# Kernel tuning notes

Hardware: AMD Instinct MI355X
Metric: run time of the kernel (lower is better)

## Reference

```python
import jax, jax.numpy as jnp
import numpy as np

B, C_IN, H, W = 16, 256, 64, 64
D, K = 128, 1024  # embed_dim, nb_entries


def setup_inputs() -> dict:
    key = jax.random.key(0)
    k1, k2, k3, k4 = jax.random.split(key, 4)
    x = jax.random.normal(k1, (B, C_IN, H, W), dtype=jnp.float32)
    conv_w = jax.random.normal(k2, (C_IN, D), dtype=jnp.float32) * 0.05
    conv_b = jax.random.normal(k3, (D,), dtype=jnp.float32) * 0.05
    embed = jax.random.normal(k4, (D, K), dtype=jnp.float32)
    return {"x": x, "conv_w": conv_w, "conv_b": conv_b, "embed": embed}


def reference(x, conv_w, conv_b, embed):
    # 1x1 conv == per-pixel matmul; go straight to NHWC layout.
    z = jnp.einsum('bchw,cd->bhwd', x, conv_w) + conv_b        # [B,H,W,D]
    flat = z.reshape(-1, D)                                     # [N,D]
    # Squared-euclidean distances to codebook columns (||f||^2 - 2 f.E + ||e||^2).
    dist = (jnp.sum(flat * flat, axis=1, keepdims=True)
            - 2.0 * (flat @ embed)
            + jnp.sum(embed * embed, axis=0, keepdims=True))    # [N,K]
    embed_ind = jnp.argmin(dist, axis=1)                        # [N] int
    embed_ind = embed_ind.reshape(B, H, W)
    quantize = jnp.take(embed.T, embed_ind, axis=0)             # [B,H,W,D] gather
    diff = jnp.mean((jax.lax.stop_gradient(quantize) - z) ** 2)
    quantize = z + jax.lax.stop_gradient(quantize - z)          # straight-through
    return quantize.transpose(0, 3, 1, 2), diff, embed_ind
```

## Files before the change

kernel.cpp:

```cpp
#include <hip/hip_runtime.h>

typedef __attribute__((ext_vector_type(4))) float f32x4;
typedef __attribute__((ext_vector_type(8))) short bf16x8;

constexpr int CIN = 256;
constexpr int D   = 128;
constexpr int K   = 1024;
constexpr int HW  = 4096;
constexpr int MT  = 128;
constexpr int DIFF_OFF = 8388608;
constexpr int IDX_OFF  = 8388609;

__device__ float g_scratch[16 + K];
__device__ __align__(16) uint4 g_efrags[64 * 4 * 64];
__device__ __align__(16) uint4 g_wfrags[8 * 8 * 3 * 64];
__device__ __align__(16) float g_embedT[K * D];

__device__ inline unsigned short f2bf(float f) {
    unsigned u = __float_as_uint(f);
    u = u + 0x7fff + ((u >> 16) & 1);
    return (unsigned short)(u >> 16);
}
__device__ inline float bf2f(unsigned short h) {
    return __uint_as_float(((unsigned)h) << 16);
}
__device__ inline void split3(float v, short& a, short& b, short& c) {
    unsigned short h = f2bf(v); float r1 = v - bf2f(h);
    unsigned short m = f2bf(r1); float r2 = r1 - bf2f(m);
    a = (short)h; b = (short)m; c = (short)f2bf(r2);
}
__device__ inline void split3t(float v, short& a, short& b, short& c) {
    unsigned u1 = __float_as_uint(v) & 0xffff0000u;
    float r1 = v - __uint_as_float(u1);
    unsigned u2 = __float_as_uint(r1) & 0xffff0000u;
    float r2 = r1 - __uint_as_float(u2);
    a = (short)(u1 >> 16); b = (short)(u2 >> 16);
    c = (short)(__float_as_uint(r2) >> 16);
}
__device__ inline float med3f(float a, float b, float c) {
    float d;
    asm("v_med3_f32 %0, %1, %2, %3" : "=v"(d) : "v"(a), "v"(b), "v"(c));
    return d;
}
__device__ inline float min3f(float a, float b, float c) {
    float d;
    asm("v_min3_f32 %0, %1, %2, %3" : "=v"(d) : "v"(a), "v"(b), "v"(c));
    return d;
}
__device__ inline float packk(float s, int kk) {
    return __uint_as_float((__float_as_uint(s) & 0xFFFFFC00u) | (unsigned)kk);
}

__device__ inline void gload_lds16(const uint4* g, uint4* l) {
    __builtin_amdgcn_global_load_lds(
        (const __attribute__((address_space(1))) unsigned int*)g,
        (__attribute__((address_space(3))) unsigned int*)l,
        16, 0, 0);
}

__global__ void vq_prep_all(const float* __restrict__ embed,
                            const float* __restrict__ conv_w) {
    const int bi = blockIdx.x;
    const int t  = threadIdx.x;
    if (bi < 128) {
        __shared__ float tile[32][33];
        int kb = bi >> 2, db = bi & 3;
        int tk = t & 31, td = t >> 5;
        #pragma unroll
        for (int dd = 0; dd < 4; ++dd)
            tile[td * 4 + dd][tk] =
                embed[(size_t)(db * 32 + td * 4 + dd) * K + kb * 32 + tk];
        __syncthreads();
        #pragma unroll
        for (int dd = 0; dd < 4; ++dd)
            g_embedT[(size_t)(kb * 32 + td * 4 + dd) * D + db * 32 + tk] =
                tile[tk][td * 4 + dd];
    } else if (bi < 192) {
        int kt = bi - 128, dc = t >> 6, l = t & 63;
        int k  = kt * 16 + (l & 15);
        int d0 = dc * 32 + (l >> 4) * 8;
        unsigned short hi[8];
        #pragma unroll
        for (int j = 0; j < 8; ++j)
            hi[j] = f2bf(embed[(size_t)(d0 + j) * K + k]);
        uint4 H;
        H.x = (unsigned)hi[0] | ((unsigned)hi[1] << 16);
        H.y = (unsigned)hi[2] | ((unsigned)hi[3] << 16);
        H.z = (unsigned)hi[4] | ((unsigned)hi[5] << 16);
        H.w = (unsigned)hi[6] | ((unsigned)hi[7] << 16);
        g_efrags[(kt * 4 + dc) * 64 + l] = H;
    } else if (bi < 208) {
        int old = (bi - 192) * 4 + (t >> 6), l = t & 63;
        int cb = old >> 3, db = old & 7;
        int c0 = cb * 32 + (l >> 4) * 8, d = db * 16 + (l & 15);
        short s1[8], s2[8], s3[8];
        #pragma unroll
        for (int j = 0; j < 8; ++j)
            split3(conv_w[(size_t)(c0 + j) * D + d], s1[j], s2[j], s3[j]);
        #pragma unroll
        for (int s = 0; s < 3; ++s) {
            const short* sp = s == 0 ? s1 : s == 1 ? s2 : s3;
            uint4 P;
            P.x = (unsigned)(unsigned short)sp[0] | ((unsigned)(unsigned short)sp[1] << 16);
            P.y = (unsigned)(unsigned short)sp[2] | ((unsigned)(unsigned short)sp[3] << 16);
            P.z = (unsigned)(unsigned short)sp[4] | ((unsigned)(unsigned short)sp[5] << 16);
            P.w = (unsigned)(unsigned short)sp[6] | ((unsigned)(unsigned short)sp[7] << 16);
            g_wfrags[((cb * 8 + db) * 3 + s) * 64 + l] = P;
        }
    } else {
        int k = (bi - 208) * 256 + t;
        if (k == 0) g_scratch[0] = 0.0f;
        float s = 0.0f;
        for (int d = 0; d < D; ++d) { float v = embed[d * K + k]; s += v * v; }
        g_scratch[16 + k] = s;
    }
}

#define MFMA(a, bb, c) __builtin_amdgcn_mfma_f32_16x16x32_bf16(a, bb, c, 0, 0, 0)

__global__ __launch_bounds__(256, 2) void vq_main(
    const float* __restrict__ x, const float* __restrict__ conv_b,
    float* __restrict__ out)
{
    __shared__ __align__(16) uint4 ebuf[4096];
    __shared__ float e2_s[K];
    __shared__ float tbuf[4 * 16 * 36];
    __shared__ int   ks_s[MT];
    __shared__ float red_s[4];

    const int t    = threadIdx.x;
    const int lane = t & 63;
    const int w    = t >> 6;
    const int wg   = blockIdx.x;
    const int n0   = wg * MT;
    const int b    = n0 >> 12;
    const int hw0  = n0 & 4095;
    const int pxb  = w * 32;
    const int lp   = lane & 15;
    const int lg   = lane >> 4;
    const float INF = __uint_as_float(0x7f800000u);

    for (int k = t; k < K; k += 256) e2_s[k] = g_scratch[16 + k];

    f32x4 Cz[2][8];
    #pragma unroll
    for (int db = 0; db < 8; ++db) {
        float bv = conv_b[db * 16 + lp];
        Cz[0][db] = (f32x4){bv, bv, bv, bv};
        Cz[1][db] = Cz[0][db];
    }
    {
        #pragma unroll
        for (int i = 0; i < 6; ++i)
            gload_lds16(&g_wfrags[(w * 6 + i) * 64 + lane], &ebuf[(w * 6 + i) * 64]);
        asm volatile("s_waitcnt vmcnt(0)" ::: "memory");
        __syncthreads();

        const float* xl = x + (size_t)b * CIN * HW + (size_t)(lg * 8) * HW
                          + hw0 + pxb + lp;
        for (int cb = 0; cb < 8; ++cb) {
            float v[2][8];
            #pragma unroll
            for (int rb = 0; rb < 2; ++rb)
                #pragma unroll
                for (int j = 0; j < 8; ++j)
                    v[rb][j] = xl[(size_t)(cb * 32 + j) * HW + rb * 16];
            if (cb < 7) {
                const uint4* wsrc = g_wfrags + (size_t)(cb + 1) * 1536;
                uint4* wdst = ebuf + ((cb + 1) & 1) * 1536;
                #pragma unroll
                for (int i = 0; i < 6; ++i)
                    gload_lds16(&wsrc[(w * 6 + i) * 64 + lane], &wdst[(w * 6 + i) * 64]);
            }
            bf16x8 X1[2], X2[2], X3[2];
            #pragma unroll
            for (int rb = 0; rb < 2; ++rb)
                #pragma unroll
                for (int j = 0; j < 8; ++j) {
                    short a, bb, c;
                    split3t(v[rb][j], a, bb, c);
                    X1[rb][j] = a; X2[rb][j] = bb; X3[rb][j] = c;
                }
            const uint4* wb = ebuf + (cb & 1) * 1536;
            #pragma unroll
            for (int db = 0; db < 8; ++db) {
                bf16x8 W1 = *(const bf16x8*)&wb[(db * 3 + 0) * 64 + lane];
                bf16x8 W2 = *(const bf16x8*)&wb[(db * 3 + 1) * 64 + lane];
                bf16x8 W3 = *(const bf16x8*)&wb[(db * 3 + 2) * 64 + lane];
                Cz[0][db] = MFMA(X1[0], W1, Cz[0][db]);
                Cz[1][db] = MFMA(X1[1], W1, Cz[1][db]);
                Cz[0][db] = MFMA(X1[0], W2, Cz[0][db]);
                Cz[1][db] = MFMA(X1[1], W2, Cz[1][db]);
                Cz[0][db] = MFMA(X2[0], W1, Cz[0][db]);
                Cz[1][db] = MFMA(X2[1], W1, Cz[1][db]);
                Cz[0][db] = MFMA(X1[0], W3, Cz[0][db]);
                Cz[1][db] = MFMA(X1[1], W3, Cz[1][db]);
                Cz[0][db] = MFMA(X2[0], W2, Cz[0][db]);
                Cz[1][db] = MFMA(X2[1], W2, Cz[1][db]);
                Cz[0][db] = MFMA(X3[0], W1, Cz[0][db]);
                Cz[1][db] = MFMA(X3[1], W1, Cz[1][db]);
            }
            asm volatile("s_waitcnt vmcnt(0)" ::: "memory");
            __syncthreads();
        }
    }

    bf16x8 A2h[2][4];
    {
        float* tb = tbuf + w * 576;
        #pragma unroll
        for (int rb = 0; rb < 2; ++rb) {
            #pragma unroll
            for (int dc = 0; dc < 4; ++dc) {
                #pragma unroll
                for (int h = 0; h < 2; ++h)
                    #pragma unroll
                    for (int r = 0; r < 4; ++r)
                        tb[(lg * 4 + r) * 36 + h * 16 + lp] = Cz[rb][dc * 2 + h][r];
                asm volatile("s_waitcnt lgkmcnt(0)" ::: "memory");
                f32x4 a0 = *(const f32x4*)&tb[lp * 36 + lg * 8];
                f32x4 a1 = *(const f32x4*)&tb[lp * 36 + lg * 8 + 4];
                #pragma unroll
                for (int j = 0; j < 8; ++j)
                    A2h[rb][dc][j] = (short)f2bf(-2.0f * (j < 4 ? a0[j] : a1[j - 4]));
                asm volatile("s_waitcnt lgkmcnt(0)" ::: "memory");
            }
        }
    }

    const uint4* gfr = g_efrags;
    {
        #pragma unroll
        for (int i = 0; i < 8; ++i)
            gload_lds16(&gfr[(w * 8 + i) * 64 + lane], &ebuf[(w * 8 + i) * 64]);
        asm volatile("s_waitcnt vmcnt(0)" ::: "memory");
        __syncthreads();
    }

    float v1[8], v2[8], v3[8], v4[8];
    #pragma unroll
    for (int q = 0; q < 8; ++q) { v1[q] = INF; v2[q] = INF; v3[q] = INF; v4[q] = INF; }

    for (int c = 0; c < 8; ++c) {
        if (c < 7) {
            const uint4* esrc = gfr + (size_t)(c + 1) * 2048;
            uint4* edst = ebuf + ((c + 1) & 1) * 2048;
            #pragma unroll
            for (int i = 0; i < 8; ++i)
                gload_lds16(&esrc[(w * 8 + i) * 64 + lane], &edst[(w * 8 + i) * 64]);
        }
        const bf16x8* eb = (const bf16x8*)&ebuf[(c & 1) * 2048];
        #pragma unroll
        for (int ktl = 0; ktl < 8; ++ktl) {
            int kt = c * 8 + ktl;
            bf16x8 Bh[4];
            #pragma unroll
            for (int dc = 0; dc < 4; ++dc)
                Bh[dc] = eb[(ktl * 4 + dc) * 64 + lane];
            float e2v = e2_s[kt * 16 + lp] + 512.0f;
            f32x4 C0 = (f32x4){e2v, e2v, e2v, e2v};
            f32x4 C1 = C0;
            __builtin_amdgcn_s_setprio(1);
            #pragma unroll
            for (int dc = 0; dc < 4; ++dc) {
                C0 = MFMA(A2h[0][dc], Bh[dc], C0);
                C1 = MFMA(A2h[1][dc], Bh[dc], C1);
            }
            __builtin_amdgcn_s_setprio(0);
            int kk = kt * 16 + lp;
            #pragma unroll
            for (int rb = 0; rb < 2; ++rb) {
                f32x4 C = rb ? C1 : C0;
                #pragma unroll
                for (int r = 0; r < 4; ++r) {
                    int q = rb * 4 + r;
                    float s = packk(C[r], kk);
                    float t1 = fminf(v1[q], s);
                    float t2 = med3f(s, v1[q], v2[q]);
                    float t3 = med3f(s, v2[q], v3[q]);
                    float t4 = med3f(s, v3[q], v4[q]);
                    v1[q] = t1; v2[q] = t2; v3[q] = t3; v4[q] = t4;
                }
            }
        }
        if (c < 7) {
            asm volatile("s_waitcnt vmcnt(0)" ::: "memory");
            __syncthreads();
        }
    }

    float dacc = 0.0f;
    #pragma unroll
    for (int q = 0; q < 8; ++q) {
        const int rb = q >> 2, r = q & 3;
        float a1 = v1[q], a2 = v2[q], a3 = v3[q], a4 = v4[q], a5 = INF, a6 = INF;
        #pragma unroll
        for (int off = 1; off < 16; off <<= 1) {
            float b1 = __shfl_xor(a1, off), b2 = __shfl_xor(a2, off);
            float b3 = __shfl_xor(a3, off), b4 = __shfl_xor(a4, off);
            float b5 = __shfl_xor(a5, off), b6 = __shfl_xor(a6, off);
            float m11 = fmaxf(a1, b1);
            float m12 = fmaxf(a1, b2), m21 = fmaxf(a2, b1);
            float m13 = fmaxf(a1, b3), m22 = fmaxf(a2, b2), m31 = fmaxf(a3, b1);
            float m14 = fmaxf(a1, b4), m23 = fmaxf(a2, b3), m32 = fmaxf(a3, b2), m41 = fmaxf(a4, b1);
            float m15 = fmaxf(a1, b5), m24 = fmaxf(a2, b4), m33 = fmaxf(a3, b3), m42 = fmaxf(a4, b2), m51 = fmaxf(a5, b1);
            float c1 = fminf(a1, b1);
            float c2 = min3f(a2, b2, m11);
            float c3 = min3f(m12, m21, fminf(a3, b3));
            float c4 = fminf(min3f(a4, b4, m13), fminf(m22, m31));
            float c5 = fminf(min3f(a5, b5, m14), min3f(m23, m32, m41));
            float c6 = fminf(fminf(min3f(a6, b6, m15), min3f(m24, m33, m42)), m51);
            a1 = c1; a2 = c2; a3 = c3; a4 = c4; a5 = c5; a6 = c6;
        }
        float cm[6] = {a1, a2, a3, a4, a5, a6};
        float bd = 0.0f; int bk = 0;
        #pragma unroll
        for (int j = 0; j < 6; ++j) {
            int kc = (int)(__float_as_uint(cm[j]) & 1023u);
            float sum = 0.0f;
            #pragma unroll
            for (int db = 0; db < 8; ++db)
                sum += Cz[rb][db][r] * g_embedT[(size_t)kc * D + db * 16 + lp];
            #pragma unroll
            for (int off = 1; off < 16; off <<= 1) sum += __shfl_xor(sum, off);
            float de = e2_s[kc] - 2.0f * sum;
            if (j == 0) { bd = de; bk = kc; }
            else {
                bool upd = (de < bd) || (de == bd && kc < bk);
                bd = upd ? de : bd;
                bk = upd ? kc : bk;
            }
        }
        #pragma unroll
        for (int db = 0; db < 8; ++db) {
            float qv = g_embedT[(size_t)bk * D + db * 16 + lp];
            float df = qv - Cz[rb][db][r];
            dacc += df * df;
        }
        if (lp == 0) {
            int px = pxb + rb * 16 + lg * 4 + r;
            ks_s[px] = bk;
            out[IDX_OFF + n0 + px] = (float)bk;
        }
    }
    #pragma unroll
    for (int off = 1; off <= 32; off <<= 1) dacc += __shfl_xor(dacc, off);
    if (lane == 0) red_s[w] = dacc;
    __syncthreads();

    {
        int px = t & 127, half = t >> 7;
        int ks = ks_s[px];
        const f32x4* ep = (const f32x4*)&g_embedT[(size_t)ks * D + half * 64];
        float* ob = out + (size_t)b * D * HW + hw0 + px;
        #pragma unroll
        for (int d4 = 0; d4 < 16; ++d4) {
            f32x4 q4 = ep[d4];
            int d = half * 64 + d4 * 4;
            #pragma unroll
            for (int cc = 0; cc < 4; ++cc)
                ob[(size_t)(d + cc) * HW] = q4[cc];
        }
    }
    if (t == 0) atomicAdd(&g_scratch[0], red_s[0] + red_s[1] + red_s[2] + red_s[3]);
}

__global__ void vq_final(float* __restrict__ out) {
    out[DIFF_OFF] = g_scratch[0] / 8388608.0f;
}

extern "C" void kernel_launch(void* const* d_in, const int* in_sizes, int n_in,
                              void* d_out, int out_size, void* d_ws, size_t ws_size,
                              hipStream_t stream) {
    const float* x      = (const float*)d_in[0];
    const float* conv_w = (const float*)d_in[1];
    const float* conv_b = (const float*)d_in[2];
    const float* embed  = (const float*)d_in[3];
    float* out = (float*)d_out;

    vq_prep_all<<<212, 256, 0, stream>>>(embed, conv_w);
    vq_main    <<<512, 256, 0, stream>>>(x, conv_b, out);
    vq_final   <<<1,   1,   0, stream>>>(out);
}
```

Measured before the change: 84.89 us.

## Halve pixel tile per block, double grid, and stream W3 fragments from global

Result: slower. 121.2 us (+42.7%).

```diff
diff --git a/kernel.cpp b/kernel.cpp
--- a/kernel.cpp
+++ b/kernel.cpp
@@ -7,7 +7,7 @@
 constexpr int D   = 128;
 constexpr int K   = 1024;
 constexpr int HW  = 4096;
-constexpr int MT  = 128;
+constexpr int MT  = 64;
 constexpr int DIFF_OFF = 8388608;
 constexpr int IDX_OFF  = 8388609;
 
@@ -118,11 +118,11 @@
 
 #define MFMA(a, bb, c) __builtin_amdgcn_mfma_f32_16x16x32_bf16(a, bb, c, 0, 0, 0)
 
-__global__ __launch_bounds__(256, 2) void vq_main(
+__global__ __launch_bounds__(256, 3) void vq_main(
     const float* __restrict__ x, const float* __restrict__ conv_b,
     float* __restrict__ out)
 {
-    __shared__ __align__(16) uint4 ebuf[4096];
+    __shared__ __align__(16) uint4 ebuf[2048];
     __shared__ float e2_s[K];
     __shared__ float tbuf[4 * 16 * 36];
     __shared__ int   ks_s[MT];
@@ -135,155 +135,140 @@
     const int n0   = wg * MT;
     const int b    = n0 >> 12;
     const int hw0  = n0 & 4095;
-    const int pxb  = w * 32;
+    const int pxb  = w * 16;
     const int lp   = lane & 15;
     const int lg   = lane >> 4;
     const float INF = __uint_as_float(0x7f800000u);
 
     for (int k = t; k < K; k += 256) e2_s[k] = g_scratch[16 + k];
 
-    f32x4 Cz[2][8];
+    f32x4 Cz[8];
     #pragma unroll
     for (int db = 0; db < 8; ++db) {
         float bv = conv_b[db * 16 + lp];
-        Cz[0][db] = (f32x4){bv, bv, bv, bv};
-        Cz[1][db] = Cz[0][db];
+        Cz[db] = (f32x4){bv, bv, bv, bv};
     }
     {
         #pragma unroll
-        for (int i = 0; i < 6; ++i)
-            gload_lds16(&g_wfrags[(w * 6 + i) * 64 + lane], &ebuf[(w * 6 + i) * 64]);
+        for (int ii = 0; ii < 4; ++ii) {
+            int bi = w * 4 + ii;
+            gload_lds16(&g_wfrags[(((bi >> 1)) * 3 + (bi & 1)) * 64 + lane],
+                        &ebuf[bi * 64]);
+        }
         asm volatile("s_waitcnt vmcnt(0)" ::: "memory");
         __syncthreads();
 
         const float* xl = x + (size_t)b * CIN * HW + (size_t)(lg * 8) * HW
                           + hw0 + pxb + lp;
         for (int cb = 0; cb < 8; ++cb) {
-            float v[2][8];
-            #pragma unroll
-            for (int rb = 0; rb < 2; ++rb)
+            float v[8];
+            #pragma unroll
+            for (int j = 0; j < 8; ++j)
+                v[j] = xl[(size_t)(cb * 32 + j) * HW];
+            if (cb < 7) {
                 #pragma unroll
-                for (int j = 0; j < 8; ++j)
-                    v[rb][j] = xl[(size_t)(cb * 32 + j) * HW + rb * 16];
-            if (cb < 7) {
-                const uint4* wsrc = g_wfrags + (size_t)(cb + 1) * 1536;
-                uint4* wdst = ebuf + ((cb + 1) & 1) * 1536;
-                #pragma unroll
-                for (int i = 0; i < 6; ++i)
-                    gload_lds16(&wsrc[(w * 6 + i) * 64 + lane], &wdst[(w * 6 + i) * 64]);
-            }
-            bf16x8 X1[2], X2[2], X3[2];
-            #pragma unroll
-            for (int rb = 0; rb < 2; ++rb)
-                #pragma unroll
-                for (int j = 0; j < 8; ++j) {
-                    short a, bb, c;
-                    split3t(v[rb][j], a, bb, c);
-                    X1[rb][j] = a; X2[rb][j] = bb; X3[rb][j] = c;
+                for (int ii = 0; ii < 4; ++ii) {
+                    int bi = w * 4 + ii;
+                    gload_lds16(&g_wfrags[(((cb + 1) * 8 + (bi >> 1)) * 3 + (bi & 1)) * 64 + lane],
+                                &ebuf[((cb + 1) & 1) * 1024 + bi * 64]);
                 }
-            const uint4* wb = ebuf + (cb & 1) * 1536;
+            }
+            bf16x8 X1, X2, X3;
+            #pragma unroll
+            for (int j = 0; j < 8; ++j) {
+                short a, bb, c;
+                split3t(v[j], a, bb, c);
+                X1[j] = a; X2[j] = bb; X3[j] = c;
+            }
+            const uint4* wb = ebuf + (cb & 1) * 1024;
+            bf16x8 W3n = *(const bf16x8*)&g_wfrags[((cb * 8 + 0) * 3 + 2) * 64 + lane];
             #pragma unroll
             for (int db = 0; db < 8; ++db) {
-                bf16x8 W1 = *(const bf16x8*)&wb[(db * 3 + 0) * 64 + lane];
-                bf16x8 W2 = *(const bf16x8*)&wb[(db * 3 + 1) * 64 + lane];
-                bf16x8 W3 = *(const bf16x8*)&wb[(db * 3 + 2) * 64 + lane];
-                Cz[0][db] = MFMA(X1[0], W1, Cz[0][db]);
-                Cz[1][db] = MFMA(X1[1], W1, Cz[1][db]);
-                Cz[0][db] = MFMA(X1[0], W2, Cz[0][db]);
-                Cz[1][db] = MFMA(X1[1], W2, Cz[1][db]);
-                Cz[0][db] = MFMA(X2[0], W1, Cz[0][db]);
-                Cz[1][db] = MFMA(X2[1], W1, Cz[1][db]);
-                Cz[0][db] = MFMA(X1[0], W3, Cz[0][db]);
-                Cz[1][db] = MFMA(X1[1], W3, Cz[1][db]);
-                Cz[0][db] = MFMA(X2[0], W2, Cz[0][db]);
-                Cz[1][db] = MFMA(X2[1], W2, Cz[1][db]);
-                Cz[0][db] = MFMA(X3[0], W1, Cz[0][db]);
-                Cz[1][db] = MFMA(X3[1], W1, Cz[1][db]);
+                bf16x8 W3 = W3n;
+                if (db < 7)
+                    W3n = *(const bf16x8*)&g_wfrags[((cb * 8 + db + 1) * 3 + 2) * 64 + lane];
+                bf16x8 W1 = *(const bf16x8*)&wb[(db * 2 + 0) * 64 + lane];
+                bf16x8 W2 = *(const bf16x8*)&wb[(db * 2 + 1) * 64 + lane];
+                Cz[db] = MFMA(X1, W1, Cz[db]);
+                Cz[db] = MFMA(X1, W2, Cz[db]);
+                Cz[db] = MFMA(X2, W1, Cz[db]);
+                Cz[db] = MFMA(X1, W3, Cz[db]);
+                Cz[db] = MFMA(X2, W2, Cz[db]);
+                Cz[db] = MFMA(X3, W1, Cz[db]);
             }
             asm volatile("s_waitcnt vmcnt(0)" ::: "memory");
             __syncthreads();
         }
     }
 
-    bf16x8 A2h[2][4];
+    bf16x8 A2h[4];
     {
         float* tb = tbuf + w * 576;
         #pragma unroll
-        for (int rb = 0; rb < 2; ++rb) {
-            #pragma unroll
-            for (int dc = 0; dc < 4; ++dc) {
+        for (int dc = 0; dc < 4; ++dc) {
+            #pragma unroll
+            for (int h = 0; h < 2; ++h)
                 #pragma unroll
-                for (int h = 0; h < 2; ++h)
-                    #pragma unroll
-                    for (int r = 0; r < 4; ++r)
-                        tb[(lg * 4 + r) * 36 + h * 16 + lp] = Cz[rb][dc * 2 + h][r];
-                asm volatile("s_waitcnt lgkmcnt(0)" ::: "memory");
-                f32x4 a0 = *(const f32x4*)&tb[lp * 36 + lg * 8];
-                f32x4 a1 = *(const f32x4*)&tb[lp * 36 + lg * 8 + 4];
-                #pragma unroll
-                for (int j = 0; j < 8; ++j)
-                    A2h[rb][dc][j] = (short)f2bf(-2.0f * (j < 4 ? a0[j] : a1[j - 4]));
-                asm volatile("s_waitcnt lgkmcnt(0)" ::: "memory");
-            }
+                for (int r = 0; r < 4; ++r)
+                    tb[(lg * 4 + r) * 36 + h * 16 + lp] = Cz[dc * 2 + h][r];
+            asm volatile("s_waitcnt lgkmcnt(0)" ::: "memory");
+            f32x4 a0 = *(const f32x4*)&tb[lp * 36 + lg * 8];
+            f32x4 a1 = *(const f32x4*)&tb[lp * 36 + lg * 8 + 4];
+            #pragma unroll
+            for (int j = 0; j < 8; ++j)
+                A2h[dc][j] = (short)f2bf(-2.0f * (j < 4 ? a0[j] : a1[j - 4]));
+            asm volatile("s_waitcnt lgkmcnt(0)" ::: "memory");
         }
     }
 
     const uint4* gfr = g_efrags;
     {
         #pragma unroll
-        for (int i = 0; i < 8; ++i)
-            gload_lds16(&gfr[(w * 8 + i) * 64 + lane], &ebuf[(w * 8 + i) * 64]);
+        for (int i = 0; i < 4; ++i)
+            gload_lds16(&gfr[w * 256 + i * 64 + lane], &ebuf[w * 256 + i * 64]);
         asm volatile("s_waitcnt vmcnt(0)" ::: "memory");
         __syncthreads();
     }
 
-    float v1[8], v2[8], v3[8], v4[8];
+    float v1[4], v2[4], v3[4], v4[4];
     #pragma unroll
-    for (int q = 0; q < 8; ++q) { v1[q] = INF; v2[q] = INF; v3[q] = INF; v4[q] = INF; }
-
-    for (int c = 0; c < 8; ++c) {
-        if (c < 7) {
-            const uint4* esrc = gfr + (size_t)(c + 1) * 2048;
-            uint4* edst = ebuf + ((c + 1) & 1) * 2048;
-            #pragma unroll
-            for (int i = 0; i < 8; ++i)
-                gload_lds16(&esrc[(w * 8 + i) * 64 + lane], &edst[(w * 8 + i) * 64]);
-        }
-        const bf16x8* eb = (const bf16x8*)&ebuf[(c & 1) * 2048];
-        #pragma unroll
-        for (int ktl = 0; ktl < 8; ++ktl) {
-            int kt = c * 8 + ktl;
+    for (int q = 0; q < 4; ++q) { v1[q] = INF; v2[q] = INF; v3[q] = INF; v4[q] = INF; }
+
+    for (int c = 0; c < 16; ++c) {
+        if (c < 15) {
+            const uint4* esrc = gfr + (size_t)(c + 1) * 1024;
+            uint4* edst = ebuf + ((c + 1) & 1) * 1024;
+            #pragma unroll
+            for (int i = 0; i < 4; ++i)
+                gload_lds16(&esrc[w * 256 + i * 64 + lane], &edst[w * 256 + i * 64]);
+        }
+        const bf16x8* eb = (const bf16x8*)&ebuf[(c & 1) * 1024];
+        #pragma unroll
+        for (int ktl = 0; ktl < 4; ++ktl) {
+            int kt = c * 4 + ktl;
             bf16x8 Bh[4];
             #pragma unroll
             for (int dc = 0; dc < 4; ++dc)
                 Bh[dc] = eb[(ktl * 4 + dc) * 64 + lane];
             float e2v = e2_s[kt * 16 + lp] + 512.0f;
             f32x4 C0 = (f32x4){e2v, e2v, e2v, e2v};
-            f32x4 C1 = C0;
             __builtin_amdgcn_s_setprio(1);
             #pragma unroll
-            for (int dc = 0; dc < 4; ++dc) {
-                C0 = MFMA(A2h[0][dc], Bh[dc], C0);
-                C1 = MFMA(A2h[1][dc], Bh[dc], C1);
-            }
+            for (int dc = 0; dc < 4; ++dc)
+                C0 = MFMA(A2h[dc], Bh[dc], C0);
             __builtin_amdgcn_s_setprio(0);
             int kk = kt * 16 + lp;
             #pragma unroll
-            for (int rb = 0; rb < 2; ++rb) {
-                f32x4 C = rb ? C1 : C0;
-                #pragma unroll
-                for (int r = 0; r < 4; ++r) {
-                    int q = rb * 4 + r;
-                    float s = packk(C[r], kk);
-                    float t1 = fminf(v1[q], s);
-                    float t2 = med3f(s, v1[q], v2[q]);
-                    float t3 = med3f(s, v2[q], v3[q]);
-                    float t4 = med3f(s, v3[q], v4[q]);
-                    v1[q] = t1; v2[q] = t2; v3[q] = t3; v4[q] = t4;
-                }
-            }
-        }
-        if (c < 7) {
+            for (int q = 0; q < 4; ++q) {
+                float s = packk(C0[q], kk);
+                float t1 = fminf(v1[q], s);
+                float t2 = med3f(s, v1[q], v2[q]);
+                float t3 = med3f(s, v2[q], v3[q]);
+                float t4 = med3f(s, v3[q], v4[q]);
+                v1[q] = t1; v2[q] = t2; v3[q] = t3; v4[q] = t4;
+            }
+        }
+        if (c < 15) {
             asm volatile("s_waitcnt vmcnt(0)" ::: "memory");
             __syncthreads();
         }
@@ -291,8 +276,7 @@
 
     float dacc = 0.0f;
     #pragma unroll
-    for (int q = 0; q < 8; ++q) {
-        const int rb = q >> 2, r = q & 3;
+    for (int q = 0; q < 4; ++q) {
         float a1 = v1[q], a2 = v2[q], a3 = v3[q], a4 = v4[q], a5 = INF, a6 = INF;
         #pragma unroll
         for (int off = 1; off < 16; off <<= 1) {
@@ -320,7 +304,7 @@
             float sum = 0.0f;
             #pragma unroll
             for (int db = 0; db < 8; ++db)
-                sum += Cz[rb][db][r] * g_embedT[(size_t)kc * D + db * 16 + lp];
+                sum += Cz[db][q] * g_embedT[(size_t)kc * D + db * 16 + lp];
             #pragma unroll
             for (int off = 1; off < 16; off <<= 1) sum += __shfl_xor(sum, off);
             float de = e2_s[kc] - 2.0f * sum;
@@ -334,11 +318,11 @@
         #pragma unroll
         for (int db = 0; db < 8; ++db) {
             float qv = g_embedT[(size_t)bk * D + db * 16 + lp];
-            float df = qv - Cz[rb][db][r];
+            float df = qv - Cz[db][q];
             dacc += df * df;
         }
         if (lp == 0) {
-            int px = pxb + rb * 16 + lg * 4 + r;
+            int px = pxb + lg * 4 + q;
             ks_s[px] = bk;
             out[IDX_OFF + n0 + px] = (float)bk;
         }
@@ -349,14 +333,14 @@
     __syncthreads();
 
     {
-        int px = t & 127, half = t >> 7;
+        int px = t & 63, quarter = t >> 6;
         int ks = ks_s[px];
-        const f32x4* ep = (const f32x4*)&g_embedT[(size_t)ks * D + half * 64];
+        const f32x4* ep = (const f32x4*)&g_embedT[(size_t)ks * D + quarter * 32];
         float* ob = out + (size_t)b * D * HW + hw0 + px;
         #pragma unroll
-        for (int d4 = 0; d4 < 16; ++d4) {
+        for (int d4 = 0; d4 < 8; ++d4) {
             f32x4 q4 = ep[d4];
-            int d = half * 64 + d4 * 4;
+            int d = quarter * 32 + d4 * 4;
             #pragma unroll
             for (int cc = 0; cc < 4; ++cc)
                 ob[(size_t)(d + cc) * HW] = q4[cc];
@@ -378,7 +362,7 @@
     const float* embed  = (const float*)d_in[3];
     float* out = (float*)d_out;
 
-    vq_prep_all<<<212, 256, 0, stream>>>(embed, conv_w);
-    vq_main    <<<512, 256, 0, stream>>>(x, conv_b, out);
-    vq_final   <<<1,   1,   0, stream>>>(out);
-}
+    vq_prep_all<<<212,  256, 0, stream>>>(embed, conv_w);
+    vq_main    <<<1024, 256, 0, stream>>>(x, conv_b, out);
+    vq_final   <<<1,    1,   0, stream>>>(out);
+}
```
